# Kernel tuning notes

Measured on AMD Instinct MI355X. Metric: run time of the kernel, lower is better.

## Reference

```python
import jax, jax.numpy as jnp
import numpy as np

N = 2048          # nodes
DIM_H = 768       # hidden dim
NUM_J = 3
T = NUM_J + 1     # t_number wavelet scales
SINGLE_OUT = DIM_H // T  # 192 (last GCNConv also 192 since 768-3*192=192)
KEEP_THRE = 1e-4  # cfg.WaveGC.keep_thre


def setup_inputs() -> dict:
    key = jax.random.key(0)
    ks = jax.random.split(key, 6)
    x = jax.random.normal(ks[0], (N, DIM_H), jnp.float32)
    # eigenvectors of a graph Laplacian are orthonormal -> O(1/sqrt(N)) entries
    eigenvector = jax.random.normal(ks[1], (N, N), jnp.float32) / np.float32(np.sqrt(N))
    filter_signals_after = jax.random.uniform(ks[2], (1, N, T), jnp.float32)
    W_gcn = jax.random.normal(ks[3], (T, DIM_H, SINGLE_OUT), jnp.float32) / np.float32(np.sqrt(DIM_H))
    b_gcn = jnp.zeros((T, SINGLE_OUT), jnp.float32)
    fusion_W = jax.random.normal(ks[4], (DIM_H, DIM_H), jnp.float32) / np.float32(np.sqrt(DIM_H))
    fusion_b = jnp.zeros((DIM_H,), jnp.float32)
    return {"x": x, "eigenvector": eigenvector, "filter_signals_after": filter_signals_after,
            "W_gcn": W_gcn, "b_gcn": b_gcn, "fusion_W": fusion_W, "fusion_b": fusion_b}


def reference(x, eigenvector, filter_signals_after, W_gcn, b_gcn, fusion_W, fusion_b):
    # curr_signals = filter_signals_after.transpose(2,1) -> [1, T, N]; drop batch dim
    sig = filter_signals_after[0].T  # [T, N]
    evc = eigenvector                # [N, N]
    outs = []
    for t in range(T):
        # filters = V @ (diag(s_t) @ V^T)  -> [N, N]
        F_t = evc @ (sig[t][:, None] * evc.T)
        # F.normalize(filters) on [1,N,N] normalizes along dim=1 (columns of the NxN matrix)
        col_norm = jnp.sqrt(jnp.sum(F_t * F_t, axis=0, keepdims=True))
        F_t = F_t / jnp.maximum(col_norm, 1e-12)
        # threshold-sparsify: keep entries with |f| > keep_thre (mask instead of nonzero())
        Fm = jnp.where(jnp.abs(F_t) > KEEP_THRE, F_t, 0.0)
        # GCNConv(normalize=False) with edge_weight: out[j] = sum_i Fm[i,j]*(xW)[i] + b
        h = jax.nn.relu(Fm.T @ (x @ W_gcn[t]) + b_gcn[t])  # dropout p=0 (eval)
        # SimpleConv (sum aggregation with edge weights): out = Fm^T @ h
        h = Fm.T @ h
        outs.append(h)
    comb = jnp.concatenate(outs, axis=-1)  # [N, DIM_H]
    return jax.nn.relu(comb @ fusion_W + fusion_b)
```

## Files before the change

kernel.cpp:

```cpp
#include <hip/hip_runtime.h>


#define NN 2048
#define NPW 4194304L

typedef _Float16 f16x8 __attribute__((ext_vector_type(8)));
typedef float f32x4  __attribute__((ext_vector_type(4)));

__device__ inline unsigned short f16_rne(float f) {
    union { _Float16 h; unsigned short u; } c;
    c.h = (_Float16)f;
    return c.u;
}

__device__ inline void load_lds16(const void* g, void* l) {
    __builtin_amdgcn_global_load_lds(
        (const __attribute__((address_space(1))) unsigned int*)(unsigned long)g,
        (__attribute__((address_space(3))) unsigned int*)(unsigned long)l,
        16, 0, 0);
}

__global__ __launch_bounds__(256, 3)
void filter_tile128(const unsigned short* __restrict__ AhB,
                    unsigned short* __restrict__ F16B, float* __restrict__ ssB,
                    long sA, int noff)
{
    __shared__ unsigned short sAh[128 * 64];
    __shared__ unsigned short sBh[128 * 64];

    const int K = NN, N = NN;
    int tid = threadIdx.x;
    int lane = tid & 63, w = tid >> 6;
    int wbase = w * 64;
    int wr = w * 32;
    int q = lane >> 4, r15 = lane & 15;

    int idx = blockIdx.x;
    int z, it_base, jt_off = 0, nrep = 1;
    bool diag;
    if (idx < noff) {
        z = idx / 120;
        int r = idx - z * 120;
        int span = 15; it_base = 0;
        while (r >= span) { r -= span; ++it_base; --span; }
        jt_off = 1 + r;
        diag = false;
    } else {
        int d = idx - noff;
        z = d >> 3;
        it_base = (d & 7) * 2;
        diag = true;
        nrep = 2;
    }

    const unsigned short* Ah = AhB + z * sA;
    unsigned short* F = F16B + (long)z * NPW;
    float* sumsq = ssB + z * NN;

    for (int rep = 0; rep < nrep; ++rep) {
        int it = it_base + rep;
        int jt = diag ? it : (it + jt_off);
        int i0 = it * 128, j0 = jt * 128;
        bool mirror = !diag;

        f32x4 acc[2][8];
        #pragma unroll
        for (int i = 0; i < 2; ++i)
            #pragma unroll
            for (int j = 0; j < 8; ++j)
                acc[i][j] = (f32x4){0.f, 0.f, 0.f, 0.f};

        for (int k0 = 0; k0 < K; k0 += 64) {
            #pragma unroll
            for (int p = 0; p < 4; ++p) {
                int c = p * 256 + wbase + lane;
                int row = c >> 3;
                int gsw = (c & 7) ^ (row & 7);
                long off = (long)(i0 + row) * K + k0 + gsw * 8;
                int ldst = (p * 256 + wbase) * 8;
                load_lds16(Ah + off, &sAh[ldst]);
            }
            if (!diag) {
                #pragma unroll
                for (int p = 0; p < 4; ++p) {
                    int c = p * 256 + wbase + lane;
                    int row = c >> 3;
                    int gsw = (c & 7) ^ (row & 7);
                    long off = (long)(j0 + row) * K + k0 + gsw * 8;
                    int ldst = (p * 256 + wbase) * 8;
                    load_lds16(Ah + off, &sBh[ldst]);
                }
            }
            __syncthreads();

            const unsigned short* bh = diag ? sAh : sBh;

            #pragma unroll
            for (int s = 0; s < 2; ++s) {
                int g = s * 4 + q;
                f16x8 fA[2], fB[8];
                #pragma unroll
                for (int f = 0; f < 2; ++f) {
                    int ra = wr + f * 16 + r15;
                    fA[f] = *(const f16x8*)&sAh[ra * 64 + ((g ^ (ra & 7)) * 8)];
                }
                #pragma unroll
                for (int f = 0; f < 8; ++f) {
                    int rb = f * 16 + r15;
                    fB[f] = *(const f16x8*)&bh[rb * 64 + ((g ^ (rb & 7)) * 8)];
                }
                #pragma unroll
                for (int fi = 0; fi < 2; ++fi)
                    #pragma unroll
                    for (int fj = 0; fj < 8; ++fj)
                        acc[fi][fj] = __builtin_amdgcn_mfma_f32_16x16x32_f16(
                            fA[fi], fB[fj], acc[fi][fj], 0, 0, 0);
            }
            __syncthreads();
        }

        #pragma unroll
        for (int fi = 0; fi < 2; ++fi)
            #pragma unroll
            for (int r = 0; r < 4; ++r) {
                float s = 0.f;
                #pragma unroll
                for (int fj = 0; fj < 8; ++fj) {
                    float v = acc[fi][fj][r];
                    s += v * v;
                }
                s += __shfl_xor(s, 1); s += __shfl_xor(s, 2);
                s += __shfl_xor(s, 4); s += __shfl_xor(s, 8);
                if (r15 == 0)
                    atomicAdd(&sumsq[i0 + wr + fi * 16 + q * 4 + r], s);
            }

        if (mirror) {
            #pragma unroll
            for (int fj = 0; fj < 8; ++fj) {
                float s = 0.f;
                #pragma unroll
                for (int fi = 0; fi < 2; ++fi)
                    #pragma unroll
                    for (int r = 0; r < 4; ++r) {
                        float v = acc[fi][fj][r];
                        s += v * v;
                    }
                s += __shfl_xor(s, 16); s += __shfl_xor(s, 32);
                if (lane < 16)
                    atomicAdd(&sumsq[j0 + fj * 16 + lane], s);
            }
        }

        #pragma unroll
        for (int fi = 0; fi < 2; ++fi)
            #pragma unroll
            for (int fj = 0; fj < 8; ++fj) {
                int col = j0 + fj * 16 + r15;
                #pragma unroll
                for (int r = 0; r < 4; ++r) {
                    int row = i0 + wr + fi * 16 + q * 4 + r;
                    unsigned short h = f16_rne(acc[fi][fj][r]);
                    F[(long)row * N + col] = h;
                    if (mirror) F[(long)col * N + row] = h;
                }
            }
    }
}

template<int BIASM, bool RELU, bool OUTF32, bool TSTORE, int SCALE, int FI>
__global__ __launch_bounds__(256, 3)
void nt_gemm(const unsigned short* __restrict__ Ah,
             const unsigned short* __restrict__ Bh,
             unsigned short* __restrict__ Ch, float* __restrict__ Cf,
             const float* __restrict__ bias, const float* __restrict__ scaleV,
             int K, int a_rows, int b_rows, int i_valid, int j_valid, int ldc,
             long sA, long sB, long sC, int sBias, int sScale)
{
    __shared__ unsigned short sAh[2][FI * 64 * 64];
    __shared__ unsigned short sBh[2][64 * 64];

    int z = blockIdx.z;
    Ah += z * sA;
    Bh += z * sB;
    if (OUTF32) Cf += z * sC; else Ch += z * sC;
    if (BIASM)  bias += (long)z * sBias;
    if (SCALE)  scaleV += (long)z * sScale;

    int i0 = blockIdx.y * (FI * 64), j0 = blockIdx.x * 64;
    int tid = threadIdx.x;
    int lane = tid & 63, w = tid >> 6;
    int wr = w * (FI * 16);
    int q = lane >> 4, r15 = lane & 15;

    auto stage = [&](int buf, int k0) {
        #pragma unroll
        for (int p = 0; p < FI * 2; ++p) {
            int c = p * 256 + tid;
            int row = c >> 3;
            int gsw = (c & 7) ^ (row & 7);
            int ra = min(i0 + row, a_rows - 1);
            int ldst = (p * 256 + tid) * 8;
            load_lds16(Ah + (long)ra * K + k0 + gsw * 8, &sAh[buf][ldst]);
        }
        #pragma unroll
        for (int p = 0; p < 2; ++p) {
            int c = p * 256 + tid;
            int row = c >> 3;
            int gsw = (c & 7) ^ (row & 7);
            int rb = min(j0 + row, b_rows - 1);
            int ldst = (p * 256 + tid) * 8;
            load_lds16(Bh + (long)rb * K + k0 + gsw * 8, &sBh[buf][ldst]);
        }
    };

    f32x4 acc[FI][4];
    #pragma unroll
    for (int i = 0; i < FI; ++i)
        #pragma unroll
        for (int j = 0; j < 4; ++j)
            acc[i][j] = (f32x4){0.f, 0.f, 0.f, 0.f};

    stage(0, 0);
    __syncthreads();

    for (int k0 = 0; k0 < K; k0 += 64) {
        int cur = (k0 >> 6) & 1;
        if (k0 + 64 < K) stage(cur ^ 1, k0 + 64);

        #pragma unroll
        for (int s = 0; s < 2; ++s) {
            int g = s * 4 + q;
            f16x8 fA[FI], fB[4];
            #pragma unroll
            for (int f = 0; f < FI; ++f) {
                int ra = wr + f * 16 + r15;
                fA[f] = *(const f16x8*)&sAh[cur][ra * 64 + ((g ^ (ra & 7)) * 8)];
            }
            #pragma unroll
            for (int f = 0; f < 4; ++f) {
                int rb = f * 16 + r15;
                fB[f] = *(const f16x8*)&sBh[cur][rb * 64 + ((g ^ (rb & 7)) * 8)];
            }
            #pragma unroll
            for (int fi = 0; fi < FI; ++fi)
                #pragma unroll
                for (int fj = 0; fj < 4; ++fj)
                    acc[fi][fj] = __builtin_amdgcn_mfma_f32_16x16x32_f16(
                        fA[fi], fB[fj], acc[fi][fj], 0, 0, 0);
        }
        __syncthreads();
    }

    #pragma unroll
    for (int fi = 0; fi < FI; ++fi)
        #pragma unroll
        for (int fj = 0; fj < 4; ++fj) {
            int col = j0 + fj * 16 + r15;
            if (col >= j_valid) continue;
            float ivc = 1.f;
            if (SCALE == 1)
                ivc = 1.f / fmaxf(sqrtf(scaleV[col]), 1e-12f);
            #pragma unroll
            for (int r = 0; r < 4; ++r) {
                int row = i0 + wr + fi * 16 + q * 4 + r;
                if (row >= i_valid) continue;
                float v = acc[fi][fj][r];
                if (SCALE == 1) v *= ivc;
                if (BIASM == 1) v += bias[row];
                if (BIASM == 2) v += bias[col];
                if (RELU) v = fmaxf(v, 0.f);
                long off = TSTORE ? ((long)col * ldc + row)
                                  : ((long)row * ldc + col);
                if (OUTF32) Cf[off] = v;
                else        Ch[off] = f16_rne(v);
            }
        }
}

__global__ __launch_bounds__(256)
void prep_all(const float* __restrict__ V, const float* __restrict__ sig,
              const float* __restrict__ x, const float* __restrict__ Wg,
              const float* __restrict__ Wf, const float* __restrict__ bg,
              unsigned short* __restrict__ A4, float* __restrict__ zs,
              float* __restrict__ bgp, unsigned short* __restrict__ xh,
              unsigned short* __restrict__ WgTh, unsigned short* __restrict__ WfTh)
{
    int b = blockIdx.x;
    int tid = threadIdx.x;
    if (b < 4096) {
        if (b < 32) zs[b * 256 + tid] = 0.f;
        if (b == 32) {
            #pragma unroll
            for (int p = 0; p < 4; ++p) {
                int i = p * 256 + tid;
                int t = i >> 8, n = i & 255;
                bgp[i] = (n < 192) ? bg[t * 192 + n] : 0.f;
            }
        }
        long idx = ((long)b * 256 + tid) * 4;
        int k = (int)(idx & (NN - 1));
        float4 v = *(const float4*)(V + idx);
        float vv[4] = {v.x, v.y, v.z, v.w};
        float4 srow[4];
        #pragma unroll
        for (int i = 0; i < 4; ++i)
            srow[i] = *(const float4*)(sig + (k + i) * 4);
        #pragma unroll
        for (int t = 0; t < 4; ++t) {
            float sq[4] = {((const float*)&srow[0])[t], ((const float*)&srow[1])[t],
                           ((const float*)&srow[2])[t], ((const float*)&srow[3])[t]};
            ushort4 hi;
            hi.x = f16_rne(vv[0] * sqrtf(sq[0]));
            hi.y = f16_rne(vv[1] * sqrtf(sq[1]));
            hi.z = f16_rne(vv[2] * sqrtf(sq[2]));
            hi.w = f16_rne(vv[3] * sqrtf(sq[3]));
            *(ushort4*)(A4 + (long)t * NPW + idx) = hi;
        }
        return;
    }
    b -= 4096;
    if (b < 1536) {
        long idx = ((long)b * 256 + tid) * 4;
        float4 v = *(const float4*)(x + idx);
        ushort4 hi;
        hi.x = f16_rne(v.x);
        hi.y = f16_rne(v.y);
        hi.z = f16_rne(v.z);
        hi.w = f16_rne(v.w);
        *(ushort4*)(xh + idx) = hi;
        return;
    }
    b -= 1536;
    if (b < 2304) {
        int zb = b / 576;
        long idx = (long)(b - zb * 576) * 256 + tid;
        int n = (int)(idx / 768), k = (int)(idx % 768);
        WgTh[(long)zb * 147456 + idx] =
            f16_rne(Wg[(long)zb * 147456 + (long)k * 192 + n]);
        return;
    }
    b -= 2304;
    {
        long idx = (long)b * 256 + tid;
        int n = (int)(idx / 768), k = (int)(idx % 768);
        WfTh[idx] = f16_rne(Wf[(long)k * 768 + n]);
    }
}

extern "C" void kernel_launch(void* const* d_in, const int* in_sizes, int n_in,
                              void* d_out, int out_size, void* d_ws, size_t ws_size,
                              hipStream_t stream)
{
    const float* x   = (const float*)d_in[0];
    const float* evc = (const float*)d_in[1];
    const float* sig = (const float*)d_in[2];
    const float* Wg  = (const float*)d_in[3];
    const float* bg  = (const float*)d_in[4];
    const float* Wf  = (const float*)d_in[5];
    const float* bf  = (const float*)d_in[6];
    float* out = (float*)d_out;

    char* w = (char*)d_ws;
    unsigned short* F16  = (unsigned short*)w;
    unsigned short* A4   = (unsigned short*)(w + 33554432L);
    unsigned short* xh   = (unsigned short*)(w + 67108864L);
    unsigned short* WgTh = (unsigned short*)(w + 70254592L);
    unsigned short* PTh  = (unsigned short*)(w + 71827456L);
    unsigned short* HTh  = (unsigned short*)(w + 74973184L);
    unsigned short* combh= (unsigned short*)(w + 78118912L);
    unsigned short* WfTh = (unsigned short*)(w + 81264640L);
    float* rowss = (float*)(w + 82444288L);
    float* bgp   = (float*)(w + 82477056L);

    prep_all<<<10240, 256, 0, stream>>>(
        evc, sig, x, Wg, Wf, bg, A4, rowss, bgp, xh, WgTh, WfTh);

    filter_tile128<<<512, 256, 0, stream>>>(A4, F16, rowss, NPW, 480);

    nt_gemm<0, false, false, false, 0, 1><<<dim3(32, 3, 4), 256, 0, stream>>>(
        WgTh, xh, PTh, nullptr, nullptr, nullptr,
        768, 192, NN, 192, NN, NN, 147456L, 0L, 393216L, 0, 0);

    nt_gemm<1, true, false, false, 1, 1><<<dim3(32, 3, 4), 256, 0, stream>>>(
        PTh, F16, HTh, nullptr, bgp, rowss,
        NN, 192, NN, 192, NN, NN, 393216L, NPW, 393216L, 256, NN);

    nt_gemm<0, false, false, true, 1, 1><<<dim3(32, 3, 4), 256, 0, stream>>>(
        HTh, F16, combh, nullptr, nullptr, rowss,
        NN, 192, NN, 192, NN, 768, 393216L, NPW, 192L, 0, NN);

    nt_gemm<2, true, true, false, 0, 2><<<dim3(12, 16, 1), 256, 0, stream>>>(
        combh, WfTh, nullptr, out, bf, nullptr,
        768, NN, 768, NN, 768, 768, 0L, 0L, 0L, 0, 0);
}
```

Before: 231.6 us.

## Split diagonal filter tiles per block, tile weight transposes via LDS, halve fusion tile

The filter kernel now gives each diagonal 128x128 tile its own block instead of two per block, raising the grid from 512 to 544 blocks so diagonal blocks no longer run twice as long as the others. The weight transposes in prep_all now go through a padded 64x64 shared-memory tile, so both global reads and writes are coalesced instead of strided, which also shrinks that kernel's grid. The fusion GEMM switches from FI=2 to FI=1 with twice as many row blocks, trading per-block reuse for more parallelism.

```diff
diff --git a/kernel.cpp b/kernel.cpp
--- a/kernel.cpp
+++ b/kernel.cpp
@@ -36,136 +36,129 @@
     int q = lane >> 4, r15 = lane & 15;
 
     int idx = blockIdx.x;
-    int z, it_base, jt_off = 0, nrep = 1;
-    bool diag;
+    int z, it, jt;
     if (idx < noff) {
         z = idx / 120;
         int r = idx - z * 120;
-        int span = 15; it_base = 0;
-        while (r >= span) { r -= span; ++it_base; --span; }
-        jt_off = 1 + r;
-        diag = false;
+        int span = 15; it = 0;
+        while (r >= span) { r -= span; ++it; --span; }
+        jt = it + 1 + r;
     } else {
         int d = idx - noff;
-        z = d >> 3;
-        it_base = (d & 7) * 2;
-        diag = true;
-        nrep = 2;
-    }
+        z = d >> 4;
+        it = d & 15;
+        jt = it;
+    }
+    int i0 = it * 128, j0 = jt * 128;
+    bool diag = (jt == it);
+    bool mirror = !diag;
 
     const unsigned short* Ah = AhB + z * sA;
     unsigned short* F = F16B + (long)z * NPW;
     float* sumsq = ssB + z * NN;
 
-    for (int rep = 0; rep < nrep; ++rep) {
-        int it = it_base + rep;
-        int jt = diag ? it : (it + jt_off);
-        int i0 = it * 128, j0 = jt * 128;
-        bool mirror = !diag;
-
-        f32x4 acc[2][8];
-        #pragma unroll
-        for (int i = 0; i < 2; ++i)
-            #pragma unroll
-            for (int j = 0; j < 8; ++j)
-                acc[i][j] = (f32x4){0.f, 0.f, 0.f, 0.f};
-
-        for (int k0 = 0; k0 < K; k0 += 64) {
+    f32x4 acc[2][8];
+    #pragma unroll
+    for (int i = 0; i < 2; ++i)
+        #pragma unroll
+        for (int j = 0; j < 8; ++j)
+            acc[i][j] = (f32x4){0.f, 0.f, 0.f, 0.f};
+
+    for (int k0 = 0; k0 < K; k0 += 64) {
+        #pragma unroll
+        for (int p = 0; p < 4; ++p) {
+            int c = p * 256 + wbase + lane;
+            int row = c >> 3;
+            int gsw = (c & 7) ^ (row & 7);
+            long off = (long)(i0 + row) * K + k0 + gsw * 8;
+            int ldst = (p * 256 + wbase) * 8;
+            load_lds16(Ah + off, &sAh[ldst]);
+        }
+        if (!diag) {
             #pragma unroll
             for (int p = 0; p < 4; ++p) {
                 int c = p * 256 + wbase + lane;
                 int row = c >> 3;
                 int gsw = (c & 7) ^ (row & 7);
-                long off = (long)(i0 + row) * K + k0 + gsw * 8;
+                long off = (long)(j0 + row) * K + k0 + gsw * 8;
                 int ldst = (p * 256 + wbase) * 8;
-                load_lds16(Ah + off, &sAh[ldst]);
-            }
-            if (!diag) {
+                load_lds16(Ah + off, &sBh[ldst]);
+            }
+        }
+        __syncthreads();
+
+        const unsigned short* bh = diag ? sAh : sBh;
+
+        #pragma unroll
+        for (int s = 0; s < 2; ++s) {
+            int g = s * 4 + q;
+            f16x8 fA[2], fB[8];
+            #pragma unroll
+            for (int f = 0; f < 2; ++f) {
+                int ra = wr + f * 16 + r15;
+                fA[f] = *(const f16x8*)&sAh[ra * 64 + ((g ^ (ra & 7)) * 8)];
+            }
+            #pragma unroll
+            for (int f = 0; f < 8; ++f) {
+                int rb = f * 16 + r15;
+                fB[f] = *(const f16x8*)&bh[rb * 64 + ((g ^ (rb & 7)) * 8)];
+            }
+            #pragma unroll
+            for (int fi = 0; fi < 2; ++fi)
                 #pragma unroll
-                for (int p = 0; p < 4; ++p) {
-                    int c = p * 256 + wbase + lane;
-                    int row = c >> 3;
-                    int gsw = (c & 7) ^ (row & 7);
-                    long off = (long)(j0 + row) * K + k0 + gsw * 8;
-                    int ldst = (p * 256 + wbase) * 8;
-                    load_lds16(Ah + off, &sBh[ldst]);
-                }
-            }
-            __syncthreads();
-
-            const unsigned short* bh = diag ? sAh : sBh;
-
-            #pragma unroll
-            for (int s = 0; s < 2; ++s) {
-                int g = s * 4 + q;
-                f16x8 fA[2], fB[8];
+                for (int fj = 0; fj < 8; ++fj)
+                    acc[fi][fj] = __builtin_amdgcn_mfma_f32_16x16x32_f16(
+                        fA[fi], fB[fj], acc[fi][fj], 0, 0, 0);
+        }
+        __syncthreads();
+    }
+
+    #pragma unroll
+    for (int fi = 0; fi < 2; ++fi)
+        #pragma unroll
+        for (int r = 0; r < 4; ++r) {
+            float s = 0.f;
+            #pragma unroll
+            for (int fj = 0; fj < 8; ++fj) {
+                float v = acc[fi][fj][r];
+                s += v * v;
+            }
+            s += __shfl_xor(s, 1); s += __shfl_xor(s, 2);
+            s += __shfl_xor(s, 4); s += __shfl_xor(s, 8);
+            if (r15 == 0)
+                atomicAdd(&sumsq[i0 + wr + fi * 16 + q * 4 + r], s);
+        }
+
+    if (mirror) {
+        #pragma unroll
+        for (int fj = 0; fj < 8; ++fj) {
+            float s = 0.f;
+            #pragma unroll
+            for (int fi = 0; fi < 2; ++fi)
                 #pragma unroll
-                for (int f = 0; f < 2; ++f) {
-                    int ra = wr + f * 16 + r15;
-                    fA[f] = *(const f16x8*)&sAh[ra * 64 + ((g ^ (ra & 7)) * 8)];
-                }
-                #pragma unroll
-                for (int f = 0; f < 8; ++f) {
-                    int rb = f * 16 + r15;
-                    fB[f] = *(const f16x8*)&bh[rb * 64 + ((g ^ (rb & 7)) * 8)];
-                }
-                #pragma unroll
-                for (int fi = 0; fi < 2; ++fi)
-                    #pragma unroll
-                    for (int fj = 0; fj < 8; ++fj)
-                        acc[fi][fj] = __builtin_amdgcn_mfma_f32_16x16x32_f16(
-                            fA[fi], fB[fj], acc[fi][fj], 0, 0, 0);
-            }
-            __syncthreads();
-        }
-
-        #pragma unroll
-        for (int fi = 0; fi < 2; ++fi)
-            #pragma unroll
-            for (int r = 0; r < 4; ++r) {
-                float s = 0.f;
-                #pragma unroll
-                for (int fj = 0; fj < 8; ++fj) {
+                for (int r = 0; r < 4; ++r) {
                     float v = acc[fi][fj][r];
                     s += v * v;
                 }
-                s += __shfl_xor(s, 1); s += __shfl_xor(s, 2);
-                s += __shfl_xor(s, 4); s += __shfl_xor(s, 8);
-                if (r15 == 0)
-                    atomicAdd(&sumsq[i0 + wr + fi * 16 + q * 4 + r], s);
-            }
-
-        if (mirror) {
-            #pragma unroll
-            for (int fj = 0; fj < 8; ++fj) {
-                float s = 0.f;
-                #pragma unroll
-                for (int fi = 0; fi < 2; ++fi)
-                    #pragma unroll
-                    for (int r = 0; r < 4; ++r) {
-                        float v = acc[fi][fj][r];
-                        s += v * v;
-                    }
-                s += __shfl_xor(s, 16); s += __shfl_xor(s, 32);
-                if (lane < 16)
-                    atomicAdd(&sumsq[j0 + fj * 16 + lane], s);
-            }
-        }
-
-        #pragma unroll
-        for (int fi = 0; fi < 2; ++fi)
-            #pragma unroll
-            for (int fj = 0; fj < 8; ++fj) {
-                int col = j0 + fj * 16 + r15;
-                #pragma unroll
-                for (int r = 0; r < 4; ++r) {
-                    int row = i0 + wr + fi * 16 + q * 4 + r;
-                    unsigned short h = f16_rne(acc[fi][fj][r]);
-                    F[(long)row * N + col] = h;
-                    if (mirror) F[(long)col * N + row] = h;
-                }
-            }
-    }
+            s += __shfl_xor(s, 16); s += __shfl_xor(s, 32);
+            if (lane < 16)
+                atomicAdd(&sumsq[j0 + fj * 16 + lane], s);
+        }
+    }
+
+    #pragma unroll
+    for (int fi = 0; fi < 2; ++fi)
+        #pragma unroll
+        for (int fj = 0; fj < 8; ++fj) {
+            int col = j0 + fj * 16 + r15;
+            #pragma unroll
+            for (int r = 0; r < 4; ++r) {
+                int row = i0 + wr + fi * 16 + q * 4 + r;
+                unsigned short h = f16_rne(acc[fi][fj][r]);
+                F[(long)row * N + col] = h;
+                if (mirror) F[(long)col * N + row] = h;
+            }
+        }
 }
 
 template<int BIASM, bool RELU, bool OUTF32, bool TSTORE, int SCALE, int FI>
@@ -286,6 +279,7 @@
               float* __restrict__ bgp, unsigned short* __restrict__ xh,
               unsigned short* __restrict__ WgTh, unsigned short* __restrict__ WfTh)
 {
+    __shared__ float tile[64][65];
     int b = blockIdx.x;
     int tid = threadIdx.x;
     if (b < 4096) {
@@ -332,19 +326,43 @@
         return;
     }
     b -= 1536;
-    if (b < 2304) {
-        int zb = b / 576;
-        long idx = (long)(b - zb * 576) * 256 + tid;
-        int n = (int)(idx / 768), k = (int)(idx % 768);
-        WgTh[(long)zb * 147456 + idx] =
-            f16_rne(Wg[(long)zb * 147456 + (long)k * 192 + n]);
+    if (b < 144) {
+        int t = b / 36, r = b - t * 36;
+        int kt = r / 3, nt = r - kt * 3;
+        const float* src = Wg + (long)t * 147456;
+        #pragma unroll
+        for (int p = 0; p < 16; ++p) {
+            int i = p * 256 + tid;
+            int kk = i >> 6, nn = i & 63;
+            tile[kk][nn] = src[(long)(kt * 64 + kk) * 192 + nt * 64 + nn];
+        }
+        __syncthreads();
+        #pragma unroll
+        for (int p = 0; p < 16; ++p) {
+            int i = p * 256 + tid;
+            int nn = i >> 6, kk = i & 63;
+            WgTh[(long)t * 147456 + (long)(nt * 64 + nn) * 768 + kt * 64 + kk] =
+                f16_rne(tile[kk][nn]);
+        }
         return;
     }
-    b -= 2304;
+    b -= 144;
     {
-        long idx = (long)b * 256 + tid;
-        int n = (int)(idx / 768), k = (int)(idx % 768);
-        WfTh[idx] = f16_rne(Wf[(long)k * 768 + n]);
+        int kt = b / 12, nt = b - kt * 12;
+        #pragma unroll
+        for (int p = 0; p < 16; ++p) {
+            int i = p * 256 + tid;
+            int kk = i >> 6, nn = i & 63;
+            tile[kk][nn] = Wf[(long)(kt * 64 + kk) * 768 + nt * 64 + nn];
+        }
+        __syncthreads();
+        #pragma unroll
+        for (int p = 0; p < 16; ++p) {
+            int i = p * 256 + tid;
+            int nn = i >> 6, kk = i & 63;
+            WfTh[(long)(nt * 64 + nn) * 768 + kt * 64 + kk] =
+                f16_rne(tile[kk][nn]);
+        }
     }
 }
 
@@ -373,10 +391,10 @@
     float* rowss = (float*)(w + 82444288L);
     float* bgp   = (float*)(w + 82477056L);
 
-    prep_all<<<10240, 256, 0, stream>>>(
+    prep_all<<<5920, 256, 0, stream>>>(
         evc, sig, x, Wg, Wf, bg, A4, rowss, bgp, xh, WgTh, WfTh);
 
-    filter_tile128<<<512, 256, 0, stream>>>(A4, F16, rowss, NPW, 480);
+    filter_tile128<<<544, 256, 0, stream>>>(A4, F16, rowss, NPW, 480);
 
     nt_gemm<0, false, false, false, 0, 1><<<dim3(32, 3, 4), 256, 0, stream>>>(
         WgTh, xh, PTh, nullptr, nullptr, nullptr,
@@ -390,7 +408,7 @@
         HTh, F16, combh, nullptr, nullptr, rowss,
         NN, 192, NN, 192, NN, 768, 393216L, NPW, 192L, 0, NN);
 
-    nt_gemm<2, true, true, false, 0, 2><<<dim3(12, 16, 1), 256, 0, stream>>>(
+    nt_gemm<2, true, true, false, 0, 1><<<dim3(12, 32, 1), 256, 0, stream>>>(
         combh, WfTh, nullptr, out, bf, nullptr,
         768, NN, 768, NN, 768, 768, 0L, 0L, 0L, 0, 0);
 }
```

New measurement: 212.4 us. 8.3% less time.
